# Performance work log

Measured on AMD Instinct MI355X. Metric: run time of the kernel, lower is better.

Reference implementation:

```python
import jax, jax.numpy as jnp
import numpy as np


def setup_inputs() -> dict:
    key = jax.random.key(0)
    k1, k2, k3, k4 = jax.random.split(key, 4)
    B, T, N, C_IN, C_OUT, K = 32, 24, 1024, 64, 64, 3
    x = jax.random.normal(k1, (B, T, N, C_IN), dtype=jnp.float32)
    Tks = jax.random.normal(k2, (K, N, N), dtype=jnp.float32)
    # kaiming-uniform-ish init scale for Theta, small uniform bias
    bound_t = float(np.sqrt(6.0 / C_IN))
    Theta = jax.random.uniform(k3, (K, C_IN, C_OUT), dtype=jnp.float32,
                               minval=-bound_t, maxval=bound_t)
    bound_b = 1.0 / float(np.sqrt(C_IN))
    bias = jax.random.uniform(k4, (K, C_OUT), dtype=jnp.float32,
                              minval=-bound_b, maxval=bound_b)
    return {"x": x, "Tks": Tks, "Theta": Theta, "bias": bias}


def reference(x, Tks, Theta, bias):
    # torch.einsum('nn,btnc->btnc', T_k, x) extracts diag(T_k) and scales x per node.
    d = jnp.diagonal(Tks, axis1=1, axis2=2)  # [K, N]
    # sum_k diag(T_k) * x @ Theta_k  -> [B, T, N, C_OUT]
    out = jnp.einsum('kn,btnc,kco->btno', d, x, Theta)
    # each bias[k] is added once -> total additive term is sum over k
    out = out + jnp.sum(bias, axis=0)
    return out
```

## Files before the change

### kernel.cpp

```cpp
#include <hip/hip_runtime.h>


#define NNODES 1024
#define TILE_ROWS 64
#define NTILES 8
#define ROWS_PER_BLOCK (TILE_ROWS * NTILES)
#define NBLOCKS (786432 / ROWS_PER_BLOCK)

#define WS_W  0
#define WS_BS (24 * 1024)
#define WS_DV (24 * 1024 + 256)

typedef __attribute__((ext_vector_type(8))) short short8;
typedef __attribute__((ext_vector_type(4))) float f32x4;
typedef __attribute__((ext_vector_type(4))) int   i32x4;

__device__ __forceinline__ unsigned short f2bf(float f) {
    union { float f; unsigned u; } v; v.f = f;
    unsigned r = v.u + 0x7FFFu + ((v.u >> 16) & 1u);
    return (unsigned short)(r >> 16);
}

__device__ __forceinline__ int cvt_pk_bf16(float lo, float hi) {
    int r;
    asm("v_cvt_pk_bf16_f32 %0, %1, %2" : "=v"(r) : "v"(lo), "v"(hi));
    return r;
}

__device__ __forceinline__ void gload_lds16(const void* g, void* l) {
    __builtin_amdgcn_global_load_lds(
        (const __attribute__((address_space(1))) void*)g,
        (__attribute__((address_space(3))) void*)l,
        16, 0, 0);
}

__global__ void cheb_prep(const float* __restrict__ Tks,
                          const float* __restrict__ Theta,
                          const float* __restrict__ bias,
                          unsigned char* __restrict__ ws) {
    const int b = blockIdx.x;
    const int l = threadIdx.x;
    if (b < 24) {
        const int kc = b >> 3, h = (b >> 2) & 1, nb = b & 3;
        const int o  = nb * 16 + (l & 15);
        const int cb = h * 32 + (l >> 4) * 8;
        unsigned short* dst = (unsigned short*)(ws + WS_W) + ((size_t)b * 64 + l) * 8;
        #pragma unroll
        for (int j = 0; j < 8; ++j)
            dst[j] = f2bf(Theta[kc * 4096 + (cb + j) * 64 + o]);
    } else if (b < 40) {
        const int n = (b - 24) * 64 + l;
        const size_t dg = (size_t)n * (NNODES + 1);
        f32x4 v;
        v[0] = Tks[dg];
        v[1] = Tks[(size_t)NNODES * NNODES + dg];
        v[2] = Tks[(size_t)2 * NNODES * NNODES + dg];
        v[3] = 0.0f;
        *((f32x4*)(ws + WS_DV) + n) = v;
    } else {
        float* bs = (float*)(ws + WS_BS);
        bs[l] = bias[l] + bias[64 + l] + bias[128 + l];
    }
}

__global__ __launch_bounds__(256) void cheb_main(
    const float* __restrict__ x,
    const unsigned char* __restrict__ ws,
    float* __restrict__ out)
{
    __shared__ float xs[2][TILE_ROWS * 64];

    const int tid  = threadIdx.x;
    const int wave = tid >> 6;
    const int lane = tid & 63;
    const int lrow = lane & 15;
    const int lgrp = lane >> 4;
    const size_t rowbase = (size_t)blockIdx.x * ROWS_PER_BLOCK;

    const unsigned short* wimg = (const unsigned short*)(ws + WS_W);
    const float*          bsum = (const float*)(ws + WS_BS);
    const f32x4*          dvec = (const f32x4*)(ws + WS_DV);

    short8 wf[3][2][4];
    #pragma unroll
    for (int kc = 0; kc < 3; ++kc)
        #pragma unroll
        for (int h = 0; h < 2; ++h)
            #pragma unroll
            for (int nb = 0; nb < 4; ++nb)
                wf[kc][h][nb] = *(const short8*)(
                    wimg + ((size_t)(((kc * 2 + h) * 4 + nb) * 64 + lane)) * 8);

    f32x4 bs4[4];
    #pragma unroll
    for (int nb = 0; nb < 4; ++nb)
        bs4[nb] = *(const f32x4*)(bsum + nb * 16 + lgrp * 4);

#define STAGE(T, B) do {                                                      \
        _Pragma("unroll")                                                     \
        for (int s = 0; s < 4; ++s) {                                         \
            const int u_ = wave * 4 + s;                                      \
            const int R_ = u_ * 4 + lgrp;                                     \
            const int c_ = (lrow * 16) ^ ((R_ & 7) << 4);                     \
            const char* g_ = (const char*)x +                                 \
                (((rowbase + (size_t)(T) * TILE_ROWS + R_) << 8) + c_);       \
            gload_lds16(g_, &xs[B][u_ * 256]);                                \
        }                                                                     \
    } while (0)

    STAGE(0, 0);
    __syncthreads();

    #pragma unroll 1
    for (int t = 0; t < NTILES; ++t) {
        const int cur = t & 1;
        if (t + 1 < NTILES) STAGE(t + 1, cur ^ 1);

        const int R = wave * 16 + lrow;
        const int m = (lrow & 7) << 4;
        const char* rowp = (const char*)&xs[cur][R * 64];
        const int c00 = (lgrp * 32) ^ m;
        const int c01 = (lgrp * 32 + 16) ^ m;
        const f32x4 x0 = *(const f32x4*)(rowp + c00);
        const f32x4 x1 = *(const f32x4*)(rowp + c01);
        const f32x4 x2 = *(const f32x4*)(rowp + 128 + c00);
        const f32x4 x3 = *(const f32x4*)(rowp + 128 + c01);

        const size_t grow = rowbase + (size_t)t * TILE_ROWS + R;
        const f32x4 dv = dvec[grow & (NNODES - 1)];

        short8 xf[3][2];
        #pragma unroll
        for (int kc = 0; kc < 3; ++kc) {
            const float dk = dv[kc];
            i32x4 r0, r1;
            r0[0] = cvt_pk_bf16(dk * x0[0], dk * x0[1]);
            r0[1] = cvt_pk_bf16(dk * x0[2], dk * x0[3]);
            r0[2] = cvt_pk_bf16(dk * x1[0], dk * x1[1]);
            r0[3] = cvt_pk_bf16(dk * x1[2], dk * x1[3]);
            r1[0] = cvt_pk_bf16(dk * x2[0], dk * x2[1]);
            r1[1] = cvt_pk_bf16(dk * x2[2], dk * x2[3]);
            r1[2] = cvt_pk_bf16(dk * x3[0], dk * x3[1]);
            r1[3] = cvt_pk_bf16(dk * x3[2], dk * x3[3]);
            xf[kc][0] = __builtin_bit_cast(short8, r0);
            xf[kc][1] = __builtin_bit_cast(short8, r1);
        }

        f32x4 acc[4] = {f32x4{0,0,0,0}, f32x4{0,0,0,0},
                        f32x4{0,0,0,0}, f32x4{0,0,0,0}};
        #pragma unroll
        for (int kc = 0; kc < 3; ++kc)
            #pragma unroll
            for (int h = 0; h < 2; ++h)
                #pragma unroll
                for (int nb = 0; nb < 4; ++nb)
                    acc[nb] = __builtin_amdgcn_mfma_f32_16x16x32_bf16(
                        wf[kc][h][nb], xf[kc][h], acc[nb], 0, 0, 0);

        float* orow = out + grow * 64;
        #pragma unroll
        for (int nb = 0; nb < 4; ++nb) {
            f32x4 o4;
            #pragma unroll
            for (int j = 0; j < 4; ++j) o4[j] = acc[nb][j] + bs4[nb][j];
            *(f32x4*)(orow + nb * 16 + lgrp * 4) = o4;
        }

        __syncthreads();
    }
#undef STAGE
}

extern "C" void kernel_launch(void* const* d_in, const int* in_sizes, int n_in,
                              void* d_out, int out_size, void* d_ws, size_t ws_size,
                              hipStream_t stream) {
    const float* x     = (const float*)d_in[0];
    const float* Tks   = (const float*)d_in[1];
    const float* Theta = (const float*)d_in[2];
    const float* bias  = (const float*)d_in[3];
    float* out = (float*)d_out;
    unsigned char* ws = (unsigned char*)d_ws;

    hipLaunchKernelGGL(cheb_prep, dim3(41), dim3(64), 0, stream,
                       Tks, Theta, bias, ws);
    hipLaunchKernelGGL(cheb_main, dim3(NBLOCKS), dim3(256), 0, stream,
                       x, ws, out);
}
```

Before: 92.43 us.

## Deepen LDS prefetch to 4 stages with manual vmcnt waits and unrolled tiles

```diff
diff --git a/kernel.cpp b/kernel.cpp
--- a/kernel.cpp
+++ b/kernel.cpp
@@ -3,8 +3,8 @@
 
 #define NNODES 1024
 #define TILE_ROWS 64
-#define NTILES 8
-#define ROWS_PER_BLOCK (TILE_ROWS * NTILES)
+#define NT 8
+#define ROWS_PER_BLOCK (TILE_ROWS * NT)
 #define NBLOCKS (786432 / ROWS_PER_BLOCK)
 
 #define WS_W  0
@@ -68,7 +68,7 @@
     const unsigned char* __restrict__ ws,
     float* __restrict__ out)
 {
-    __shared__ float xs[2][TILE_ROWS * 64];
+    __shared__ float xs[4][TILE_ROWS * 64];
 
     const int tid  = threadIdx.x;
     const int wave = tid >> 6;
@@ -96,7 +96,12 @@
     for (int nb = 0; nb < 4; ++nb)
         bs4[nb] = *(const f32x4*)(bsum + nb * 16 + lgrp * 4);
 
-#define STAGE(T, B) do {                                                      \
+    f32x4 dvr[NT];
+    #pragma unroll
+    for (int t = 0; t < NT; ++t)
+        dvr[t] = dvec[(rowbase + t * TILE_ROWS + wave * 16 + lrow) & (NNODES - 1)];
+
+#define STAGE(T) do { if ((T) < NT) {                                         \
         _Pragma("unroll")                                                     \
         for (int s = 0; s < 4; ++s) {                                         \
             const int u_ = wave * 4 + s;                                      \
@@ -104,71 +109,74 @@
             const int c_ = (lrow * 16) ^ ((R_ & 7) << 4);                     \
             const char* g_ = (const char*)x +                                 \
                 (((rowbase + (size_t)(T) * TILE_ROWS + R_) << 8) + c_);       \
-            gload_lds16(g_, &xs[B][u_ * 256]);                                \
+            gload_lds16(g_, &xs[(T) & 3][u_ * 256]);                          \
+        } } } while (0)
+
+#define WAITV(N) do {                                                         \
+        asm volatile("s_waitcnt vmcnt(" #N ")" ::: "memory");                 \
+        __builtin_amdgcn_sched_barrier(0);                                    \
+    } while (0)
+
+#define BODY(T) do {                                                          \
+        const int R = wave * 16 + lrow;                                       \
+        const int m_ = (lrow & 7) << 4;                                       \
+        const char* rowp = (const char*)&xs[(T) & 3][R * 64];                 \
+        const int c00 = (lgrp * 32) ^ m_;                                     \
+        const int c01 = (lgrp * 32 + 16) ^ m_;                                \
+        const f32x4 x0 = *(const f32x4*)(rowp + c00);                         \
+        const f32x4 x1 = *(const f32x4*)(rowp + c01);                         \
+        const f32x4 x2 = *(const f32x4*)(rowp + 128 + c00);                   \
+        const f32x4 x3 = *(const f32x4*)(rowp + 128 + c01);                   \
+        const f32x4 dv = dvr[T];                                              \
+        short8 xf[3][2];                                                      \
+        _Pragma("unroll")                                                     \
+        for (int kc = 0; kc < 3; ++kc) {                                      \
+            const float dk = dv[kc];                                          \
+            i32x4 r0, r1;                                                     \
+            r0[0] = cvt_pk_bf16(dk * x0[0], dk * x0[1]);                      \
+            r0[1] = cvt_pk_bf16(dk * x0[2], dk * x0[3]);                      \
+            r0[2] = cvt_pk_bf16(dk * x1[0], dk * x1[1]);                      \
+            r0[3] = cvt_pk_bf16(dk * x1[2], dk * x1[3]);                      \
+            r1[0] = cvt_pk_bf16(dk * x2[0], dk * x2[1]);                      \
+            r1[1] = cvt_pk_bf16(dk * x2[2], dk * x2[3]);                      \
+            r1[2] = cvt_pk_bf16(dk * x3[0], dk * x3[1]);                      \
+            r1[3] = cvt_pk_bf16(dk * x3[2], dk * x3[3]);                      \
+            xf[kc][0] = __builtin_bit_cast(short8, r0);                       \
+            xf[kc][1] = __builtin_bit_cast(short8, r1);                       \
+        }                                                                     \
+        f32x4 acc[4] = {f32x4{0,0,0,0}, f32x4{0,0,0,0},                       \
+                        f32x4{0,0,0,0}, f32x4{0,0,0,0}};                      \
+        _Pragma("unroll")                                                     \
+        for (int kc = 0; kc < 3; ++kc)                                        \
+            _Pragma("unroll")                                                 \
+            for (int h = 0; h < 2; ++h)                                       \
+                _Pragma("unroll")                                             \
+                for (int nb = 0; nb < 4; ++nb)                                \
+                    acc[nb] = __builtin_amdgcn_mfma_f32_16x16x32_bf16(        \
+                        wf[kc][h][nb], xf[kc][h], acc[nb], 0, 0, 0);          \
+        float* orow = out + (rowbase + (size_t)(T) * TILE_ROWS + R) * 64;     \
+        _Pragma("unroll")                                                     \
+        for (int nb = 0; nb < 4; ++nb) {                                      \
+            f32x4 o4;                                                         \
+            _Pragma("unroll")                                                 \
+            for (int j = 0; j < 4; ++j) o4[j] = acc[nb][j] + bs4[nb][j];      \
+            *(f32x4*)(orow + nb * 16 + lgrp * 4) = o4;                        \
         }                                                                     \
     } while (0)
 
-    STAGE(0, 0);
-    __syncthreads();
+    STAGE(0); STAGE(1); STAGE(2);
+    STAGE(3);  WAITV(12); BODY(0);
+    STAGE(4);  WAITV(16); BODY(1);
+    STAGE(5);  WAITV(20); BODY(2);
+    STAGE(6);  WAITV(24); BODY(3);
+    STAGE(7);  WAITV(24); BODY(4);
+    STAGE(8);  WAITV(20); BODY(5);
+    STAGE(9);  WAITV(16); BODY(6);
+    STAGE(10); WAITV(12); BODY(7);
 
-    #pragma unroll 1
-    for (int t = 0; t < NTILES; ++t) {
-        const int cur = t & 1;
-        if (t + 1 < NTILES) STAGE(t + 1, cur ^ 1);
-
-        const int R = wave * 16 + lrow;
-        const int m = (lrow & 7) << 4;
-        const char* rowp = (const char*)&xs[cur][R * 64];
-        const int c00 = (lgrp * 32) ^ m;
-        const int c01 = (lgrp * 32 + 16) ^ m;
-        const f32x4 x0 = *(const f32x4*)(rowp + c00);
-        const f32x4 x1 = *(const f32x4*)(rowp + c01);
-        const f32x4 x2 = *(const f32x4*)(rowp + 128 + c00);
-        const f32x4 x3 = *(const f32x4*)(rowp + 128 + c01);
-
-        const size_t grow = rowbase + (size_t)t * TILE_ROWS + R;
-        const f32x4 dv = dvec[grow & (NNODES - 1)];
-
-        short8 xf[3][2];
-        #pragma unroll
-        for (int kc = 0; kc < 3; ++kc) {
-            const float dk = dv[kc];
-            i32x4 r0, r1;
-            r0[0] = cvt_pk_bf16(dk * x0[0], dk * x0[1]);
-            r0[1] = cvt_pk_bf16(dk * x0[2], dk * x0[3]);
-            r0[2] = cvt_pk_bf16(dk * x1[0], dk * x1[1]);
-            r0[3] = cvt_pk_bf16(dk * x1[2], dk * x1[3]);
-            r1[0] = cvt_pk_bf16(dk * x2[0], dk * x2[1]);
-            r1[1] = cvt_pk_bf16(dk * x2[2], dk * x2[3]);
-            r1[2] = cvt_pk_bf16(dk * x3[0], dk * x3[1]);
-            r1[3] = cvt_pk_bf16(dk * x3[2], dk * x3[3]);
-            xf[kc][0] = __builtin_bit_cast(short8, r0);
-            xf[kc][1] = __builtin_bit_cast(short8, r1);
-        }
-
-        f32x4 acc[4] = {f32x4{0,0,0,0}, f32x4{0,0,0,0},
-                        f32x4{0,0,0,0}, f32x4{0,0,0,0}};
-        #pragma unroll
-        for (int kc = 0; kc < 3; ++kc)
-            #pragma unroll
-            for (int h = 0; h < 2; ++h)
-                #pragma unroll
-                for (int nb = 0; nb < 4; ++nb)
-                    acc[nb] = __builtin_amdgcn_mfma_f32_16x16x32_bf16(
-                        wf[kc][h][nb], xf[kc][h], acc[nb], 0, 0, 0);
-
-        float* orow = out + grow * 64;
-        #pragma unroll
-        for (int nb = 0; nb < 4; ++nb) {
-            f32x4 o4;
-            #pragma unroll
-            for (int j = 0; j < 4; ++j) o4[j] = acc[nb][j] + bs4[nb][j];
-            *(f32x4*)(orow + nb * 16 + lgrp * 4) = o4;
-        }
-
-        __syncthreads();
-    }
 #undef STAGE
+#undef WAITV
+#undef BODY
 }
 
 extern "C" void kernel_launch(void* const* d_in, const int* in_sizes, int n_in,
```

Result: slower. 95.81 us (+3.7%).
